# Kernel optimization log

Measured on AMD Instinct MI355X. Metric: run time of the kernel, lower is better.

The kernel has to match this reference:

```python
import jax, jax.numpy as jnp
import numpy as np

DECAY = 0.9


def setup_inputs() -> dict:
    key = jax.random.key(0)
    k1, k2, k3 = jax.random.split(key, 3)
    B, S, D, M = 4, 4096, 1024, 4096
    x = jax.random.normal(k1, (B, S, D), dtype=jnp.float32)
    w1 = jax.random.normal(k2, (M, D), dtype=jnp.float32) * (1.0 / np.sqrt(D))
    w2 = jax.random.normal(k3, (D, M), dtype=jnp.float32) * (1.0 / np.sqrt(M))
    return {"x": x, "w1": w1, "w2": w2}


def reference(x, w1, w2):
    B, S, D = x.shape
    idx = jnp.arange(S)
    diff = idx[:, None] - idx[None, :]          # [S, S]
    mask = diff >= 0
    # clamp negative exponents before pow to avoid inf, then mask
    d = jnp.where(mask, diff, 0).astype(x.dtype)
    decay_matrix = (DECAY ** d) * (1.0 - DECAY) * mask.astype(x.dtype)  # [S, S]
    # causal exponential-decay EMA as dense matmul: current[b,t] = sum_s dm[t,s] x[b,s]
    current_states = jnp.einsum('ts,bsd->btd', decay_matrix, x)
    # roll by 1 with zeroed first step
    previous_states = jnp.concatenate(
        [jnp.zeros_like(current_states[:, :1]), current_states[:, :-1]], axis=1)
    # MemoryMLP: w2(silu(w1(prev)))
    h = jax.nn.silu(jnp.einsum('btd,md->btm', previous_states, w1))
    mem_out = jnp.einsum('btm,dm->btd', h, w2)
    final_state = current_states[:, -1, :]
    surprise_loss = jnp.mean((mem_out - jax.lax.stop_gradient(x)) ** 2)
    return mem_out, surprise_loss, final_state
```

## Files before the change

### kernel.cpp

```cpp
#include <hip/hip_runtime.h>
#include <hip/hip_bf16.h>
#include <stdint.h>

#define BSZ 4
#define SEQ 4096
#define DIM 1024
#define MDIM 4096
#define DECAYF 0.9f
#define OMD 0.1f
#define CHUNK 128
#define NCHUNK 32
#define DECAY_CHUNK 1.3901844577868923e-06f

typedef __bf16 bf16_t;
typedef __bf16 bf16x8 __attribute__((ext_vector_type(8)));
typedef __bf16 bf16x4 __attribute__((ext_vector_type(4)));
typedef float floatx4 __attribute__((ext_vector_type(4)));

__device__ __forceinline__ void load16_lds(const void* g, void* l) {
  __builtin_amdgcn_global_load_lds(
      (__attribute__((address_space(1))) void*)g,
      (__attribute__((address_space(3))) void*)l,
      16, 0, 0);
}

#define SB()  __builtin_amdgcn_sched_barrier(0)
#define BAR() __builtin_amdgcn_s_barrier()
#define WAIT_LGKM0() do { asm volatile("s_waitcnt lgkmcnt(0)"); SB(); } while (0)

__global__ void scan_chunk_kernel(const float* __restrict__ x,
                                  float* __restrict__ chunk_end) {
  int t = blockIdx.x * 256 + threadIdx.x;
  int d = t & (DIM - 1);
  int c = (t >> 10) & (NCHUNK - 1);
  int b = t >> 15;
  const float* xp = x + ((size_t)(b * SEQ + c * CHUNK + 64)) * DIM + d;
  float p = 0.f;
#pragma unroll 8
  for (int s = 0; s < 64; ++s) p = DECAYF * p + OMD * xp[(size_t)s * DIM];
  chunk_end[t] = p;
}

__global__ void scan_carry_kernel(const float* __restrict__ chunk_end,
                                  float* __restrict__ carry_in,
                                  float* __restrict__ final_state) {
  int t = blockIdx.x * 256 + threadIdx.x;
  int d = t & (DIM - 1);
  int b = t >> 10;
  float carry = 0.f;
#pragma unroll
  for (int c = 0; c < NCHUNK; ++c) {
    int idx = (b * NCHUNK + c) * DIM + d;
    carry_in[idx] = carry;
    carry = carry * DECAY_CHUNK + chunk_end[idx];
  }
  final_state[t] = carry;
}

__global__ void scan_emit_kernel(const float* __restrict__ x,
                                 const float* __restrict__ carry_in,
                                 bf16_t* __restrict__ prev) {
  int t = blockIdx.x * 256 + threadIdx.x;
  int d = t & (DIM - 1);
  int c = (t >> 10) & (NCHUNK - 1);
  int b = t >> 15;
  size_t base = ((size_t)(b * SEQ + c * CHUNK)) * DIM + d;
  const float* xp = x + base;
  bf16_t* pp = prev + base;
  float cs = carry_in[t];
#pragma unroll 4
  for (int s = 0; s < CHUNK; ++s) {
    pp[(size_t)s * DIM] = (bf16_t)cs;
    cs = DECAYF * cs + OMD * xp[(size_t)s * DIM];
  }
}

__global__ void cvt_bf16_kernel(const float* __restrict__ w, bf16_t* __restrict__ o) {
  int t = blockIdx.x * 256 + threadIdx.x;
  float4 v = ((const float4*)w)[t];
  bf16x4 r = { (bf16_t)v.x, (bf16_t)v.y, (bf16_t)v.z, (bf16_t)v.w };
  ((bf16x4*)o)[t] = r;
}

#define READ_A(dst, CA, MH)                                                    \
  _Pragma("unroll") for (int i_ = 0; i_ < 4; ++i_)                             \
      _Pragma("unroll") for (int k_ = 0; k_ < 2; ++k_)                         \
          dst[i_][k_] = *(const bf16x8*)((const char*)(CA) + wrBase +          \
                                         (MH) * 8192 + i_ * 2048 + rbase +     \
                                         ((k_ * 64 + kc) ^ lswz));

#define READ_B(dst, CB, NH)                                                    \
  _Pragma("unroll") for (int j_ = 0; j_ < 2; ++j_)                             \
      _Pragma("unroll") for (int k_ = 0; k_ < 2; ++k_)                         \
          dst[j_][k_] = *(const bf16x8*)((const char*)(CB) + wcBase +          \
                                         (NH) * 4096 + j_ * 2048 + rbase +     \
                                         ((k_ * 64 + kc) ^ lswz));

#define MMQ(AF, BF, MO, NO)                                                    \
  _Pragma("unroll") for (int k_ = 0; k_ < 2; ++k_)                             \
      _Pragma("unroll") for (int i_ = 0; i_ < 4; ++i_)                         \
          _Pragma("unroll") for (int j_ = 0; j_ < 2; ++j_)                     \
              acc[(MO) + i_][(NO) + j_] =                                      \
                  __builtin_amdgcn_mfma_f32_16x16x32_bf16(                     \
                      AF[i_][k_], BF[j_][k_], acc[(MO) + i_][(NO) + j_],       \
                      0, 0, 0);

template <int N, int K, int MT, int EPI>
__global__ __launch_bounds__(512, 2) void gemm256_kernel(
    const bf16_t* __restrict__ A, const bf16_t* __restrict__ B,
    void* __restrict__ Cout, const float* __restrict__ X,
    float* __restrict__ loss_acc) {
  constexpr int NT = N / 256;
  constexpr int NTK = K / 64;
  static_assert((NTK & 1) == 0 && NTK >= 4, "even K-tile count");
  static_assert(MT % 8 == 0, "m-tiles divisible by XCD count");
  __shared__ __attribute__((aligned(16))) bf16_t sA[2][16384];
  __shared__ __attribute__((aligned(16))) bf16_t sB[2][16384];

  const int tid = threadIdx.x;
  const int wave = tid >> 6;
  const int lane = tid & 63;
  const int bid = blockIdx.x;
  const int xcd = bid & 7;
  const int slot = bid >> 3;
  const int tm = (xcd * (MT / 8) + slot / NT) * 256;
  const int tn = (slot % NT) * 256;
  const int wr = wave >> 2;
  const int wc = wave & 3;
  const int wrBase = wr * 16384;
  const int wcBase = wc * 8192;
  const int rbase = (lane & 15) * 128;
  const int kc = (lane >> 4) * 16;
  const int lswz = ((lane >> 1) & 7) << 4;
  const int srow = wave * 8 + (lane >> 3);
  const int scolb = ((lane & 7) * 16) ^ (((srow >> 1) & 7) << 4);

  floatx4 acc[8][4];
#pragma unroll
  for (int i = 0; i < 8; ++i)
#pragma unroll
    for (int j = 0; j < 4; ++j) acc[i][j] = (floatx4){0.f, 0.f, 0.f, 0.f};

  auto stage_ht = [&](const bf16_t* G, int tb, bf16_t* lbuf, int kt, int h) {
    char* lbase = (char*)lbuf + h * 16384 + wave * 1024;
    const char* gbase =
        (const char*)G + ((size_t)(tb + h * 128 + srow) * K + kt) * 2 + scolb;
    load16_lds(gbase, lbase);
    load16_lds(gbase + (size_t)64 * K * 2, lbase + 8192);
  };

  auto tile4 = [&](int t, bf16_t* cA, bf16_t* cB, bf16_t* nB) {
    bf16x8 a0[4][2], a1[4][2], b0[2][2], b1[2][2];
    const int kt2 = (t + 2) * 64;
    READ_A(a0, cA, 0);
    READ_B(b0, cB, 0);
    if (t + 1 < NTK) stage_ht(B, tn, nB, (t + 1) * 64, 1);
    SB(); BAR();
    WAIT_LGKM0();
    __builtin_amdgcn_s_setprio(1);
    MMQ(a0, b0, 0, 0);
    __builtin_amdgcn_s_setprio(0);
    SB(); BAR();
    READ_A(a1, cA, 1);
    SB(); BAR();
    WAIT_LGKM0();
    __builtin_amdgcn_s_setprio(1);
    MMQ(a1, b0, 4, 0);
    __builtin_amdgcn_s_setprio(0);
    SB(); BAR();
    READ_B(b1, cB, 1);
    if (t + 2 < NTK) {
      stage_ht(A, tm, cA, kt2, 0);
      stage_ht(A, tm, cA, kt2, 1);
    }
    SB(); BAR();
    WAIT_LGKM0();
    __builtin_amdgcn_s_setprio(1);
    MMQ(a1, b1, 4, 2);
    __builtin_amdgcn_s_setprio(0);
    SB(); BAR();
    if (t + 2 < NTK) stage_ht(B, tn, cB, kt2, 0);
    SB(); BAR();
    __builtin_amdgcn_s_setprio(1);
    MMQ(a0, b1, 0, 2);
    __builtin_amdgcn_s_setprio(0);
    SB();
    if (t + 1 < NTK) {
      if (t + 2 < NTK) { asm volatile("s_waitcnt vmcnt(6)"); SB(); }
      else             { asm volatile("s_waitcnt vmcnt(0)"); SB(); }
    }
    BAR();
  };

  stage_ht(A, tm, sA[0], 0, 0);
  stage_ht(A, tm, sA[0], 0, 1);
  stage_ht(B, tn, sB[0], 0, 0);
  stage_ht(B, tn, sB[0], 0, 1);
  stage_ht(A, tm, sA[1], 64, 0);
  stage_ht(A, tm, sA[1], 64, 1);
  stage_ht(B, tn, sB[1], 64, 0);
  asm volatile("s_waitcnt vmcnt(6)");
  SB(); BAR();

#pragma unroll 1
  for (int t = 0; t < NTK; t += 2) {
    tile4(t, sA[0], sB[0], sB[1]);
    tile4(t + 1, sA[1], sB[1], sB[0]);
  }

  const int r0 = (lane >> 4) * 4;
  const int cn = lane & 15;
  if constexpr (EPI == 0) {
    bf16_t* H = (bf16_t*)Cout;
#pragma unroll
    for (int i = 0; i < 8; ++i)
#pragma unroll
      for (int j = 0; j < 4; ++j)
#pragma unroll
        for (int r = 0; r < 4; ++r) {
          int m = tm + wr * 128 + i * 16 + r0 + r;
          int n = tn + wc * 64 + j * 16 + cn;
          float v = acc[i][j][r];
          v = v / (1.f + __expf(-v));
          H[(size_t)m * N + n] = (bf16_t)v;
        }
  } else {
    float* O = (float*)Cout;
    float ls = 0.f;
#pragma unroll
    for (int i = 0; i < 8; ++i)
#pragma unroll
      for (int j = 0; j < 4; ++j)
#pragma unroll
        for (int r = 0; r < 4; ++r) {
          int m = tm + wr * 128 + i * 16 + r0 + r;
          int n = tn + wc * 64 + j * 16 + cn;
          size_t off = (size_t)m * N + n;
          float v = acc[i][j][r];
          O[off] = v;
          float dd = v - X[off];
          ls += dd * dd;
        }
#pragma unroll
    for (int s = 32; s > 0; s >>= 1) ls += __shfl_down(ls, s, 64);
    if (lane == 0) atomicAdd(loss_acc, ls);
  }
}

#undef READ_A
#undef READ_B
#undef MMQ

__global__ void finalize_loss_kernel(const float* __restrict__ loss_acc,
                                     float* __restrict__ out) {
  if (threadIdx.x == 0)
    out[0] = loss_acc[0] * (1.0f / (float)(BSZ * SEQ * DIM));
}

extern "C" void kernel_launch(void* const* d_in, const int* in_sizes, int n_in,
                              void* d_out, int out_size, void* d_ws, size_t ws_size,
                              hipStream_t stream) {
  const float* x  = (const float*)d_in[0];
  const float* w1 = (const float*)d_in[1];
  const float* w2 = (const float*)d_in[2];
  float* out = (float*)d_out;

  const int BT = BSZ * SEQ;
  char* ws = (char*)d_ws;
  bf16_t* prev      = (bf16_t*)(ws);
  bf16_t* h         = (bf16_t*)(ws + 33554432ull);
  bf16_t* w1b       = (bf16_t*)(ws + 167772160ull);
  bf16_t* w2b       = (bf16_t*)(ws + 176160768ull);
  float*  chunk_end = (float*)(ws + 184549376ull);
  float*  carry_in  = (float*)(ws + 185073664ull);
  float*  loss_acc  = (float*)(ws + 185597952ull);

  hipMemsetAsync(loss_acc, 0, sizeof(float), stream);

  cvt_bf16_kernel<<<4096, 256, 0, stream>>>(w1, w1b);
  cvt_bf16_kernel<<<4096, 256, 0, stream>>>(w2, w2b);

  scan_chunk_kernel<<<(BSZ * NCHUNK * DIM) / 256, 256, 0, stream>>>(x, chunk_end);
  scan_carry_kernel<<<(BSZ * DIM) / 256, 256, 0, stream>>>(chunk_end, carry_in,
                                                           out + 16777217);
  scan_emit_kernel<<<(BSZ * NCHUNK * DIM) / 256, 256, 0, stream>>>(x, carry_in, prev);

  gemm256_kernel<MDIM, DIM, BT / 256, 0>
      <<<(BT / 256) * (MDIM / 256), 512, 0, stream>>>(prev, w1b, h, nullptr, nullptr);

  gemm256_kernel<DIM, MDIM, BT / 256, 1>
      <<<(BT / 256) * (DIM / 256), 512, 0, stream>>>(h, w2b, out, x, loss_acc);

  finalize_loss_kernel<<<1, 64, 0, stream>>>(loss_acc, out + 16777216);
}
```

Before: 474.7 us.

## Software-pipeline LDS fragment reads across K-tiles and drop explicit lgkm waits

Restructures the GEMM main loop so the first A/B register fragments of the next K-tile are read from LDS during the last MFMA block of the current tile, hoisting fragment registers out of the per-tile lambda. The barriers and lgkmcnt(0) waits are reduced from five phases to four, and the B-stage prefetch is merged with the A stage. This aims to hide LDS read latency behind MFMA work and cut barrier stalls. The cost is more live registers (both fragment sets persist across iterations), plus reliance on compiler-inserted waits for LDS reads, which could serialize or be fragile around the buffer reuse.

```diff
diff --git a/kernel.cpp b/kernel.cpp
--- a/kernel.cpp
+++ b/kernel.cpp
@@ -26,7 +26,6 @@
 
 #define SB()  __builtin_amdgcn_sched_barrier(0)
 #define BAR() __builtin_amdgcn_s_barrier()
-#define WAIT_LGKM0() do { asm volatile("s_waitcnt lgkmcnt(0)"); SB(); } while (0)
 
 __global__ void scan_chunk_kernel(const float* __restrict__ x,
                                   float* __restrict__ chunk_end) {
@@ -141,6 +140,8 @@
 #pragma unroll
     for (int j = 0; j < 4; ++j) acc[i][j] = (floatx4){0.f, 0.f, 0.f, 0.f};
 
+  bf16x8 a0[4][2], a1[4][2], b0[2][2], b1[2][2];
+
   auto stage_ht = [&](const bf16_t* G, int tb, bf16_t* lbuf, int kt, int h) {
     char* lbase = (char*)lbuf + h * 16384 + wave * 1024;
     const char* gbase =
@@ -149,47 +150,43 @@
     load16_lds(gbase + (size_t)64 * K * 2, lbase + 8192);
   };
 
-  auto tile4 = [&](int t, bf16_t* cA, bf16_t* cB, bf16_t* nB) {
-    bf16x8 a0[4][2], a1[4][2], b0[2][2], b1[2][2];
+  auto tileR = [&](int t, bf16_t* cA, bf16_t* cB, bf16_t* nA, bf16_t* nB) {
     const int kt2 = (t + 2) * 64;
-    READ_A(a0, cA, 0);
-    READ_B(b0, cB, 0);
+    READ_A(a1, cA, 1);
     if (t + 1 < NTK) stage_ht(B, tn, nB, (t + 1) * 64, 1);
-    SB(); BAR();
-    WAIT_LGKM0();
+    SB();
     __builtin_amdgcn_s_setprio(1);
     MMQ(a0, b0, 0, 0);
-    __builtin_amdgcn_s_setprio(0);
-    SB(); BAR();
-    READ_A(a1, cA, 1);
-    SB(); BAR();
-    WAIT_LGKM0();
-    __builtin_amdgcn_s_setprio(1);
-    MMQ(a1, b0, 4, 0);
     __builtin_amdgcn_s_setprio(0);
     SB(); BAR();
     READ_B(b1, cB, 1);
+    SB();
+    __builtin_amdgcn_s_setprio(1);
+    MMQ(a1, b0, 4, 0);
+    __builtin_amdgcn_s_setprio(0);
+    SB(); BAR();
     if (t + 2 < NTK) {
       stage_ht(A, tm, cA, kt2, 0);
       stage_ht(A, tm, cA, kt2, 1);
+      stage_ht(B, tn, cB, kt2, 0);
     }
+    SB();
+    __builtin_amdgcn_s_setprio(1);
+    MMQ(a0, b1, 0, 2);
+    __builtin_amdgcn_s_setprio(0);
+    SB();
+    if (t + 2 < NTK) { asm volatile("s_waitcnt vmcnt(6)"); }
+    else             { asm volatile("s_waitcnt vmcnt(0)"); }
     SB(); BAR();
-    WAIT_LGKM0();
+    if (t + 1 < NTK) {
+      READ_A(a0, nA, 0);
+      READ_B(b0, nB, 0);
+    }
+    SB();
     __builtin_amdgcn_s_setprio(1);
     MMQ(a1, b1, 4, 2);
     __builtin_amdgcn_s_setprio(0);
-    SB(); BAR();
-    if (t + 2 < NTK) stage_ht(B, tn, cB, kt2, 0);
-    SB(); BAR();
-    __builtin_amdgcn_s_setprio(1);
-    MMQ(a0, b1, 0, 2);
-    __builtin_amdgcn_s_setprio(0);
-    SB();
-    if (t + 1 < NTK) {
-      if (t + 2 < NTK) { asm volatile("s_waitcnt vmcnt(6)"); SB(); }
-      else             { asm volatile("s_waitcnt vmcnt(0)"); SB(); }
-    }
-    BAR();
+    SB();
   };
 
   stage_ht(A, tm, sA[0], 0, 0);
@@ -201,11 +198,14 @@
   stage_ht(B, tn, sB[1], 64, 0);
   asm volatile("s_waitcnt vmcnt(6)");
   SB(); BAR();
+  READ_A(a0, sA[0], 0);
+  READ_B(b0, sB[0], 0);
+  SB();
 
 #pragma unroll 1
   for (int t = 0; t < NTK; t += 2) {
-    tile4(t, sA[0], sB[0], sB[1]);
-    tile4(t + 1, sA[1], sB[1], sB[0]);
+    tileR(t, sA[0], sB[0], sA[1], sB[1]);
+    tileR(t + 1, sA[1], sB[1], sA[0], sB[0]);
   }
 
   const int r0 = (lane >> 4) * 4;
```

Measured after the change: 506.3 us. 1.07x slower.
